# Performance work log

Measured on AMD Instinct MI355X. Metric: run time of the kernel, lower is better.

The kernel has to match this reference:

```python
import jax, jax.numpy as jnp
import numpy as np

B, N, EMBED, CHEB_K, INP, HID = 32, 8192, 16, 2, 2, 64


def setup_inputs() -> dict:
    key = jax.random.key(0)
    k1, k2, k3, k4 = jax.random.split(key, 4)
    return {
        "x": jax.random.normal(k1, (B, N, INP), dtype=jnp.float32),
        "adj": jax.random.normal(k2, (N, EMBED), dtype=jnp.float32),
        "weights_pool": jax.random.normal(k3, (EMBED, CHEB_K, INP, HID), dtype=jnp.float32) * 0.1,
        "bias_pool": jax.random.normal(k4, (EMBED, HID), dtype=jnp.float32) * 0.1,
    }


def reference(x, adj, weights_pool, bias_pool):
    n = adj.shape[0]
    cheb_k = weights_pool.shape[1]
    # adaptive adjacency: row-softmax of relu(E E^T)
    ADJ = jax.nn.softmax(jax.nn.relu(adj @ adj.T), axis=1)  # [n, n]
    support_set = [jnp.eye(n, dtype=x.dtype), ADJ]
    for k in range(2, cheb_k):  # Chebyshev recursion (fixed small k)
        support_set.append(2.0 * ADJ @ support_set[-1] - support_set[-2])
    supports = jnp.stack(support_set, axis=0)  # [k, n, n]
    # node-adaptive weights / bias
    weights = jnp.einsum("nd,dkio->nkio", adj, weights_pool)  # [n,k,inp,hid]
    bias = adj @ bias_pool  # [n, hid]
    # graph propagation, directly in bnkc layout (fuses the permute)
    x_g = jnp.einsum("knm,bmc->bnkc", supports, x)  # [b,n,k,inp]
    out = jnp.einsum("bnki,nkio->bno", x_g, weights) + bias  # [b,n,hid]
    return out
```

## Files before the change

kernel.cpp:

```cpp
#include <hip/hip_runtime.h>

#define NN 8192
#define BB 32
#define EMB 16
#define HID 64

typedef __attribute__((ext_vector_type(8))) short bf16x8;
typedef __attribute__((ext_vector_type(4))) float f32x4;

static __device__ inline unsigned short f2b(float f) {
    union { float f; unsigned u; } v; v.f = f;
    return (unsigned short)((v.u + 0x7fffu + ((v.u >> 16) & 1u)) >> 16);
}

static __device__ inline unsigned packbf(unsigned e_even, unsigned e_odd) {
#if __has_builtin(__builtin_amdgcn_perm)
    return __builtin_amdgcn_perm(e_odd, e_even, 0x07060302u);
#else
    return (e_odd & 0xFFFF0000u) | (e_even >> 16);
#endif
}

__global__ void k_build(const float* __restrict__ x, const float* __restrict__ adj,
                        const float* __restrict__ wp, const float* __restrict__ bp,
                        short* __restrict__ VTf, short* __restrict__ Afrag,
                        short* __restrict__ adjS, unsigned short* __restrict__ WbufB) {
    const int t = threadIdx.x;
    const int bx = blockIdx.x;
    if (bx < 256) {
        const int c = bx;
        const int u = t >> 6, lane = t & 63, l = lane & 15, q = lane >> 4;
        const int j = 16 * u + l, b = j >> 1, ch = j & 1;
        const int m0 = 32 * c + 8 * q;
        const float* xp = x + (size_t)b * (NN * 2) + m0 * 2;
        uint4 d;
        unsigned dd[4];
#pragma unroll
        for (int i = 0; i < 4; ++i) {
            float4 xx = *(const float4*)(xp + 4 * i);
            float v0 = ch ? xx.y : xx.x;
            float v1 = ch ? xx.w : xx.z;
            dd[i] = (unsigned)f2b(v0) | ((unsigned)f2b(v1) << 16);
        }
        d.x = dd[0]; d.y = dd[1]; d.z = dd[2]; d.w = dd[3];
        *(uint4*)(VTf + ((size_t)(c * 4 + u) * 64 + lane) * 8) = d;
    } else if (bx < 384) {
        const int cc = t >> 7, tt = t & 127;
        const int c = (bx - 256) * 2 + cc;
        const int h = tt >> 6, lane = tt & 63, l = lane & 15, q = lane >> 4;
        const int row = 32 * c + 8 * (l >> 2) + (l & 3) + 4 * h;
        const float* ap = adj + (size_t)row * EMB + (q & 1) * 8;
        float4 a0 = *(const float4*)(ap);
        float4 a1 = *(const float4*)(ap + 4);
        uint4 d;
        d.x = (unsigned)f2b(a0.x) | ((unsigned)f2b(a0.y) << 16);
        d.y = (unsigned)f2b(a0.z) | ((unsigned)f2b(a0.w) << 16);
        d.z = (unsigned)f2b(a1.x) | ((unsigned)f2b(a1.y) << 16);
        d.w = (unsigned)f2b(a1.z) | ((unsigned)f2b(a1.w) << 16);
        *(uint4*)(Afrag + ((size_t)(c * 2 + h) * 64 + lane) * 8) = d;
    } else if (bx < 512) {
        const float L2E = 1.4426950408889634f;
        int idx = (bx - 384) * 256 + t;
        float4 aa = *(const float4*)(adj + (size_t)idx * 4);
        uint2 us;
        us.x = (unsigned)f2b(aa.x * L2E) | ((unsigned)f2b(aa.y * L2E) << 16);
        us.y = (unsigned)f2b(aa.z * L2E) | ((unsigned)f2b(aa.w * L2E) << 16);
        *(uint2*)(adjS + (size_t)idx * 4) = us;
    } else {
        const int nl = t >> 4, og = t & 15;
        const int n = (bx - 512) * 16 + nl;
        const float4* wp4 = (const float4*)wp;
        const float4* bp4 = (const float4*)bp;
        float an[EMB];
#pragma unroll
        for (int d = 0; d < EMB; ++d) an[d] = adj[n * EMB + d];
        float4 w[5];
#pragma unroll
        for (int c = 0; c < 5; ++c) { w[c].x = w[c].y = w[c].z = w[c].w = 0.f; }
#pragma unroll
        for (int d = 0; d < EMB; ++d) {
            float a = an[d];
#pragma unroll
            for (int c = 0; c < 4; ++c) {
                float4 p = wp4[(d * 4 + c) * 16 + og];
                w[c].x += a * p.x; w[c].y += a * p.y; w[c].z += a * p.z; w[c].w += a * p.w;
            }
            float4 pb = bp4[d * 16 + og];
            w[4].x += a * pb.x; w[4].y += a * pb.y; w[4].z += a * pb.z; w[4].w += a * pb.w;
        }
#pragma unroll
        for (int c = 0; c < 5; ++c) {
            ushort4 pk;
            pk.x = f2b(w[c].x); pk.y = f2b(w[c].y); pk.z = f2b(w[c].z); pk.w = f2b(w[c].w);
            *(ushort4*)(WbufB + (size_t)n * 320 + c * 64 + og * 4) = pk;
        }
    }
}

__launch_bounds__(512, 1)
__global__ void k_fused(const short* __restrict__ Afrag, const short* __restrict__ adjS,
                        const short* __restrict__ VTf,
                        const unsigned short* __restrict__ WbufB, const float* __restrict__ x,
                        float* __restrict__ out) {
    const int t = threadIdx.x;
    const int wv = t >> 6;
    const int lane = t & 63;
    const int l = lane & 15;
    const int q = lane >> 4;
    const int n0 = blockIdx.x * 32;
    const int cbeg = wv * 32;
    const int cend = cbeg + 32;

    __shared__ __align__(16) unsigned short ysl[8][32][68];
    __shared__ float dsl[8][32];
    __shared__ float xl[32][68];
    __shared__ float ylf[32][68];

    bf16x8 Bn[2];
    bf16x8 zv = {0, 0, 0, 0, 0, 0, 0, 0};
#pragma unroll
    for (int s = 0; s < 2; ++s) {
        const short* src = adjS + (size_t)(n0 + 16 * s + l) * EMB + (q & 1) * 8;
        bf16x8 v = *(const bf16x8*)src;
        Bn[s] = (q < 2) ? v : zv;
    }
    const short one = (short)0x3F80;
    bf16x8 ones = {one, one, one, one, one, one, one, one};

    f32x4 acc[4][2];
    f32x4 dacc[2];
#pragma unroll
    for (int u = 0; u < 4; ++u)
#pragma unroll
        for (int s = 0; s < 2; ++s) { acc[u][s][0] = acc[u][s][1] = acc[u][s][2] = acc[u][s][3] = 0.f; }
#pragma unroll
    for (int s = 0; s < 2; ++s) { dacc[s][0] = dacc[s][1] = dacc[s][2] = dacc[s][3] = 0.f; }

    const short* Ap = Afrag + (size_t)lane * 8;
    const short* Vp = VTf + (size_t)lane * 8;

    bf16x8 aCur0 = *(const bf16x8*)(Ap + (size_t)cbeg * 1024);
    bf16x8 aCur1 = *(const bf16x8*)(Ap + (size_t)cbeg * 1024 + 512);

    for (int cg = cbeg; cg < cend; ++cg) {
        bf16x8 v0 = *(const bf16x8*)(Vp + (size_t)cg * 2048);
        bf16x8 v1 = *(const bf16x8*)(Vp + (size_t)cg * 2048 + 512);
        bf16x8 v2 = *(const bf16x8*)(Vp + (size_t)cg * 2048 + 1024);
        bf16x8 v3 = *(const bf16x8*)(Vp + (size_t)cg * 2048 + 1536);
        const int cgn = (cg + 1 < cend) ? cg + 1 : cbeg;
        bf16x8 aN0 = *(const bf16x8*)(Ap + (size_t)cgn * 1024);
        bf16x8 aN1 = *(const bf16x8*)(Ap + (size_t)cgn * 1024 + 512);

        f32x4 z = {0.f, 0.f, 0.f, 0.f};
        f32x4 S0[2], S1[2];
#pragma unroll
        for (int s = 0; s < 2; ++s) {
            S0[s] = __builtin_amdgcn_mfma_f32_16x16x32_bf16(aCur0, Bn[s], z, 0, 0, 0);
            S1[s] = __builtin_amdgcn_mfma_f32_16x16x32_bf16(aCur1, Bn[s], z, 0, 0, 0);
        }
#pragma unroll
        for (int s = 0; s < 2; ++s) {
            unsigned w0[4], w1[4];
#pragma unroll
            for (int r = 0; r < 4; ++r) {
                union { float f; unsigned u; } p0, p1;
                p0.f = __builtin_amdgcn_exp2f(fmaxf(S0[s][r], 0.f));
                p1.f = __builtin_amdgcn_exp2f(fmaxf(S1[s][r], 0.f));
                w0[r] = p0.u;
                w1[r] = p1.u;
            }
            union { bf16x8 v; unsigned d[4]; } pf;
            pf.d[0] = packbf(w0[0], w0[1]);
            pf.d[1] = packbf(w0[2], w0[3]);
            pf.d[2] = packbf(w1[0], w1[1]);
            pf.d[3] = packbf(w1[2], w1[3]);
            acc[0][s] = __builtin_amdgcn_mfma_f32_16x16x32_bf16(v0, pf.v, acc[0][s], 0, 0, 0);
            acc[1][s] = __builtin_amdgcn_mfma_f32_16x16x32_bf16(v1, pf.v, acc[1][s], 0, 0, 0);
            acc[2][s] = __builtin_amdgcn_mfma_f32_16x16x32_bf16(v2, pf.v, acc[2][s], 0, 0, 0);
            acc[3][s] = __builtin_amdgcn_mfma_f32_16x16x32_bf16(v3, pf.v, acc[3][s], 0, 0, 0);
            dacc[s] = __builtin_amdgcn_mfma_f32_16x16x32_bf16(ones, pf.v, dacc[s], 0, 0, 0);
        }
        aCur0 = aN0;
        aCur1 = aN1;
    }

#pragma unroll
    for (int s = 0; s < 2; ++s) {
        const int nl_w = 16 * s + l;
#pragma unroll
        for (int u = 0; u < 4; ++u) {
            union { float f; unsigned u; } a0, a1, a2, a3;
            a0.f = acc[u][s][0]; a1.f = acc[u][s][1]; a2.f = acc[u][s][2]; a3.f = acc[u][s][3];
            uint2 pk;
            pk.x = packbf(a0.u, a1.u);
            pk.y = packbf(a2.u, a3.u);
            *(uint2*)&ysl[wv][nl_w][16 * u + 4 * q] = pk;
        }
        if (q == 0) dsl[wv][nl_w] = dacc[s][0];
    }
    __syncthreads();

    const int nl = t >> 4, og = t & 15;
    const int n = n0 + nl;

    float4 W[5];
#pragma unroll
    for (int c = 0; c < 5; ++c) {
        ushort4 pw = *(const ushort4*)(WbufB + (size_t)n * 320 + c * 64 + og * 4);
        union { unsigned u; float f; } c0, c1, c2, c3;
        c0.u = (unsigned)pw.x << 16; c1.u = (unsigned)pw.y << 16;
        c2.u = (unsigned)pw.z << 16; c3.u = (unsigned)pw.w << 16;
        W[c].x = c0.f; W[c].y = c1.f; W[c].z = c2.f; W[c].w = c3.f;
    }

    float4 ysum; ysum.x = ysum.y = ysum.z = ysum.w = 0.f;
    float dsum = 0.f;
#pragma unroll
    for (int s = 0; s < 8; ++s) {
        ushort4 p = *(const ushort4*)&ysl[s][nl][og * 4];
        union { unsigned u; float f; } c0, c1, c2, c3;
        c0.u = (unsigned)p.x << 16; c1.u = (unsigned)p.y << 16;
        c2.u = (unsigned)p.z << 16; c3.u = (unsigned)p.w << 16;
        ysum.x += c0.f; ysum.y += c1.f; ysum.z += c2.f; ysum.w += c3.f;
        dsum += dsl[s][nl];
    }
    float rden = 1.f / dsum;
    *(float4*)&ylf[nl][og * 4] = make_float4(ysum.x * rden, ysum.y * rden, ysum.z * rden, ysum.w * rden);

    float2 x0 = *(const float2*)(x + ((size_t)(og * 2) * NN + n) * 2);
    float2 x1 = *(const float2*)(x + ((size_t)(og * 2 + 1) * NN + n) * 2);
    xl[nl][og * 4 + 0] = x0.x; xl[nl][og * 4 + 1] = x0.y;
    xl[nl][og * 4 + 2] = x1.x; xl[nl][og * 4 + 3] = x1.y;
    __syncthreads();

#pragma unroll 4
    for (int b = 0; b < BB; ++b) {
        float xb0 = xl[nl][2 * b], xb1 = xl[nl][2 * b + 1];
        float yb0 = ylf[nl][2 * b], yb1 = ylf[nl][2 * b + 1];
        f32x4 o4;
        o4[0] = xb0 * W[0].x + xb1 * W[1].x + yb0 * W[2].x + yb1 * W[3].x + W[4].x;
        o4[1] = xb0 * W[0].y + xb1 * W[1].y + yb0 * W[2].y + yb1 * W[3].y + W[4].y;
        o4[2] = xb0 * W[0].z + xb1 * W[1].z + yb0 * W[2].z + yb1 * W[3].z + W[4].z;
        o4[3] = xb0 * W[0].w + xb1 * W[1].w + yb0 * W[2].w + yb1 * W[3].w + W[4].w;
        __builtin_nontemporal_store(o4, (f32x4*)(out + ((size_t)b * NN + n) * HID + og * 4));
    }
}

extern "C" void kernel_launch(void* const* d_in, const int* in_sizes, int n_in,
                              void* d_out, int out_size, void* d_ws, size_t ws_size,
                              hipStream_t stream) {
    const float* x   = (const float*)d_in[0];
    const float* adj = (const float*)d_in[1];
    const float* wp  = (const float*)d_in[2];
    const float* bp  = (const float*)d_in[3];
    float* out = (float*)d_out;

    char* w = (char*)d_ws;
    short* VTf   = (short*)w;
    short* Afrag = VTf + (size_t)256 * 4 * 64 * 8;
    short* adjS  = Afrag + (size_t)256 * 2 * 64 * 8;
    unsigned short* WbufB = (unsigned short*)(adjS + (size_t)NN * EMB);

    k_build<<<1024, 256, 0, stream>>>(x, adj, wp, bp, VTf, Afrag, adjS, WbufB);
    k_fused<<<NN / 32, 512, 0, stream>>>(Afrag, adjS, VTf, WbufB, x, out);
}
```

Before: 116.5 us.

## Split attention over key halves with 64-node tiles and separate epilogue kernel

```diff
diff --git a/kernel.cpp b/kernel.cpp
--- a/kernel.cpp
+++ b/kernel.cpp
@@ -22,9 +22,8 @@
 }
 
 __global__ void k_build(const float* __restrict__ x, const float* __restrict__ adj,
-                        const float* __restrict__ wp, const float* __restrict__ bp,
                         short* __restrict__ VTf, short* __restrict__ Afrag,
-                        short* __restrict__ adjS, unsigned short* __restrict__ WbufB) {
+                        short* __restrict__ adjS) {
     const int t = threadIdx.x;
     const int bx = blockIdx.x;
     if (bx < 256) {
@@ -58,7 +57,7 @@
         d.z = (unsigned)f2b(a1.x) | ((unsigned)f2b(a1.y) << 16);
         d.w = (unsigned)f2b(a1.z) | ((unsigned)f2b(a1.w) << 16);
         *(uint4*)(Afrag + ((size_t)(c * 2 + h) * 64 + lane) * 8) = d;
-    } else if (bx < 512) {
+    } else {
         const float L2E = 1.4426950408889634f;
         int idx = (bx - 384) * 256 + t;
         float4 aa = *(const float4*)(adj + (size_t)idx * 4);
@@ -66,60 +65,31 @@
         us.x = (unsigned)f2b(aa.x * L2E) | ((unsigned)f2b(aa.y * L2E) << 16);
         us.y = (unsigned)f2b(aa.z * L2E) | ((unsigned)f2b(aa.w * L2E) << 16);
         *(uint2*)(adjS + (size_t)idx * 4) = us;
-    } else {
-        const int nl = t >> 4, og = t & 15;
-        const int n = (bx - 512) * 16 + nl;
-        const float4* wp4 = (const float4*)wp;
-        const float4* bp4 = (const float4*)bp;
-        float an[EMB];
-#pragma unroll
-        for (int d = 0; d < EMB; ++d) an[d] = adj[n * EMB + d];
-        float4 w[5];
-#pragma unroll
-        for (int c = 0; c < 5; ++c) { w[c].x = w[c].y = w[c].z = w[c].w = 0.f; }
-#pragma unroll
-        for (int d = 0; d < EMB; ++d) {
-            float a = an[d];
-#pragma unroll
-            for (int c = 0; c < 4; ++c) {
-                float4 p = wp4[(d * 4 + c) * 16 + og];
-                w[c].x += a * p.x; w[c].y += a * p.y; w[c].z += a * p.z; w[c].w += a * p.w;
-            }
-            float4 pb = bp4[d * 16 + og];
-            w[4].x += a * pb.x; w[4].y += a * pb.y; w[4].z += a * pb.z; w[4].w += a * pb.w;
-        }
-#pragma unroll
-        for (int c = 0; c < 5; ++c) {
-            ushort4 pk;
-            pk.x = f2b(w[c].x); pk.y = f2b(w[c].y); pk.z = f2b(w[c].z); pk.w = f2b(w[c].w);
-            *(ushort4*)(WbufB + (size_t)n * 320 + c * 64 + og * 4) = pk;
-        }
     }
 }
 
 __launch_bounds__(512, 1)
-__global__ void k_fused(const short* __restrict__ Afrag, const short* __restrict__ adjS,
-                        const short* __restrict__ VTf,
-                        const unsigned short* __restrict__ WbufB, const float* __restrict__ x,
-                        float* __restrict__ out) {
+__global__ void k_main(const short* __restrict__ Afrag, const short* __restrict__ adjS,
+                       const short* __restrict__ VTf,
+                       float* __restrict__ gnum, float* __restrict__ gden) {
     const int t = threadIdx.x;
     const int wv = t >> 6;
     const int lane = t & 63;
     const int l = lane & 15;
     const int q = lane >> 4;
-    const int n0 = blockIdx.x * 32;
-    const int cbeg = wv * 32;
-    const int cend = cbeg + 32;
-
-    __shared__ __align__(16) unsigned short ysl[8][32][68];
-    __shared__ float dsl[8][32];
-    __shared__ float xl[32][68];
-    __shared__ float ylf[32][68];
-
-    bf16x8 Bn[2];
+    const int tile = blockIdx.x & 127;
+    const int mh = blockIdx.x >> 7;
+    const int n0 = tile * 64;
+    const int cbeg = mh * 128 + wv * 16;
+    const int cend = cbeg + 16;
+
+    __shared__ __align__(16) unsigned short ysl[8][64][68];
+    __shared__ float dsl[8][64];
+
+    bf16x8 Bn[4];
     bf16x8 zv = {0, 0, 0, 0, 0, 0, 0, 0};
 #pragma unroll
-    for (int s = 0; s < 2; ++s) {
+    for (int s = 0; s < 4; ++s) {
         const short* src = adjS + (size_t)(n0 + 16 * s + l) * EMB + (q & 1) * 8;
         bf16x8 v = *(const bf16x8*)src;
         Bn[s] = (q < 2) ? v : zv;
@@ -127,14 +97,14 @@
     const short one = (short)0x3F80;
     bf16x8 ones = {one, one, one, one, one, one, one, one};
 
-    f32x4 acc[4][2];
-    f32x4 dacc[2];
+    f32x4 acc[4][4];
+    f32x4 dacc[4];
 #pragma unroll
     for (int u = 0; u < 4; ++u)
 #pragma unroll
-        for (int s = 0; s < 2; ++s) { acc[u][s][0] = acc[u][s][1] = acc[u][s][2] = acc[u][s][3] = 0.f; }
-#pragma unroll
-    for (int s = 0; s < 2; ++s) { dacc[s][0] = dacc[s][1] = dacc[s][2] = dacc[s][3] = 0.f; }
+        for (int s = 0; s < 4; ++s) { acc[u][s][0] = acc[u][s][1] = acc[u][s][2] = acc[u][s][3] = 0.f; }
+#pragma unroll
+    for (int s = 0; s < 4; ++s) { dacc[s][0] = dacc[s][1] = dacc[s][2] = dacc[s][3] = 0.f; }
 
     const short* Ap = Afrag + (size_t)lane * 8;
     const short* Vp = VTf + (size_t)lane * 8;
@@ -152,14 +122,14 @@
         bf16x8 aN1 = *(const bf16x8*)(Ap + (size_t)cgn * 1024 + 512);
 
         f32x4 z = {0.f, 0.f, 0.f, 0.f};
-        f32x4 S0[2], S1[2];
-#pragma unroll
-        for (int s = 0; s < 2; ++s) {
+        f32x4 S0[4], S1[4];
+#pragma unroll
+        for (int s = 0; s < 4; ++s) {
             S0[s] = __builtin_amdgcn_mfma_f32_16x16x32_bf16(aCur0, Bn[s], z, 0, 0, 0);
             S1[s] = __builtin_amdgcn_mfma_f32_16x16x32_bf16(aCur1, Bn[s], z, 0, 0, 0);
         }
 #pragma unroll
-        for (int s = 0; s < 2; ++s) {
+        for (int s = 0; s < 4; ++s) {
             unsigned w0[4], w1[4];
 #pragma unroll
             for (int r = 0; r < 4; ++r) {
@@ -185,7 +155,7 @@
     }
 
 #pragma unroll
-    for (int s = 0; s < 2; ++s) {
+    for (int s = 0; s < 4; ++s) {
         const int nl_w = 16 * s + l;
 #pragma unroll
         for (int u = 0; u < 4; ++u) {
@@ -200,38 +170,80 @@
     }
     __syncthreads();
 
+    float* gn = gnum + (size_t)(mh * 128 + tile) * 64 * 64;
+    float* gd = gden + (size_t)(mh * 128 + tile) * 64;
     const int nl = t >> 4, og = t & 15;
+#pragma unroll
+    for (int h = 0; h < 2; ++h) {
+        const int nr = nl + 32 * h;
+        f32x4 ysum = {0.f, 0.f, 0.f, 0.f};
+        float dsum = 0.f;
+#pragma unroll
+        for (int s = 0; s < 8; ++s) {
+            ushort4 p = *(const ushort4*)&ysl[s][nr][og * 4];
+            union { unsigned u; float f; } c0, c1, c2, c3;
+            c0.u = (unsigned)p.x << 16; c1.u = (unsigned)p.y << 16;
+            c2.u = (unsigned)p.z << 16; c3.u = (unsigned)p.w << 16;
+            ysum[0] += c0.f; ysum[1] += c1.f; ysum[2] += c2.f; ysum[3] += c3.f;
+            dsum += dsl[s][nr];
+        }
+        *(f32x4*)(gn + (size_t)nr * 64 + og * 4) = ysum;
+        if (og == 0) gd[nr] = dsum;
+    }
+}
+
+__global__ void k_epi2(const float* __restrict__ adj, const float* __restrict__ wp,
+                       const float* __restrict__ bp, const float* __restrict__ x,
+                       const float* __restrict__ gnum, const float* __restrict__ gden,
+                       float* __restrict__ out) {
+    const int t = threadIdx.x;
+    const int nl = t >> 4, og = t & 15;
+    const int tile = blockIdx.x >> 1;
+    const int half = blockIdx.x & 1;
+    const int n0 = blockIdx.x * 32;
+    const int nloc = half * 32 + nl;
     const int n = n0 + nl;
 
+    __shared__ float wpl[EMB][5][64];
+    __shared__ float adjl[32][EMB];
+    __shared__ float xl[32][68];
+    __shared__ float ylf[32][68];
+
+    for (int i = t; i < EMB * 5 * 64; i += 512) {
+        const int d = i / 320, r = i % 320, c = r >> 6, j = r & 63;
+        wpl[d][c][j] = (c < 4) ? wp[(size_t)(d * 4 + c) * 64 + j] : bp[(size_t)d * 64 + j];
+    }
+    adjl[nl][og] = adj[(size_t)(n0 + nl) * EMB + og];
+
+    const float* gn0 = gnum + (size_t)tile * 64 * 64;
+    const float* gn1 = gnum + (size_t)(128 + tile) * 64 * 64;
+    f32x4 y0 = *(const f32x4*)(gn0 + (size_t)nloc * 64 + og * 4);
+    f32x4 y1 = *(const f32x4*)(gn1 + (size_t)nloc * 64 + og * 4);
+    float dsum = gden[(size_t)tile * 64 + nloc] + gden[(size_t)(128 + tile) * 64 + nloc];
+    float rden = 1.f / dsum;
+    ylf[nl][og * 4 + 0] = (y0[0] + y1[0]) * rden;
+    ylf[nl][og * 4 + 1] = (y0[1] + y1[1]) * rden;
+    ylf[nl][og * 4 + 2] = (y0[2] + y1[2]) * rden;
+    ylf[nl][og * 4 + 3] = (y0[3] + y1[3]) * rden;
+
+    float2 x0 = *(const float2*)(x + ((size_t)(og * 2) * NN + n) * 2);
+    float2 x1v = *(const float2*)(x + ((size_t)(og * 2 + 1) * NN + n) * 2);
+    xl[nl][og * 4 + 0] = x0.x; xl[nl][og * 4 + 1] = x0.y;
+    xl[nl][og * 4 + 2] = x1v.x; xl[nl][og * 4 + 3] = x1v.y;
+    __syncthreads();
+
     float4 W[5];
 #pragma unroll
-    for (int c = 0; c < 5; ++c) {
-        ushort4 pw = *(const ushort4*)(WbufB + (size_t)n * 320 + c * 64 + og * 4);
-        union { unsigned u; float f; } c0, c1, c2, c3;
-        c0.u = (unsigned)pw.x << 16; c1.u = (unsigned)pw.y << 16;
-        c2.u = (unsigned)pw.z << 16; c3.u = (unsigned)pw.w << 16;
-        W[c].x = c0.f; W[c].y = c1.f; W[c].z = c2.f; W[c].w = c3.f;
-    }
-
-    float4 ysum; ysum.x = ysum.y = ysum.z = ysum.w = 0.f;
-    float dsum = 0.f;
-#pragma unroll
-    for (int s = 0; s < 8; ++s) {
-        ushort4 p = *(const ushort4*)&ysl[s][nl][og * 4];
-        union { unsigned u; float f; } c0, c1, c2, c3;
-        c0.u = (unsigned)p.x << 16; c1.u = (unsigned)p.y << 16;
-        c2.u = (unsigned)p.z << 16; c3.u = (unsigned)p.w << 16;
-        ysum.x += c0.f; ysum.y += c1.f; ysum.z += c2.f; ysum.w += c3.f;
-        dsum += dsl[s][nl];
-    }
-    float rden = 1.f / dsum;
-    *(float4*)&ylf[nl][og * 4] = make_float4(ysum.x * rden, ysum.y * rden, ysum.z * rden, ysum.w * rden);
-
-    float2 x0 = *(const float2*)(x + ((size_t)(og * 2) * NN + n) * 2);
-    float2 x1 = *(const float2*)(x + ((size_t)(og * 2 + 1) * NN + n) * 2);
-    xl[nl][og * 4 + 0] = x0.x; xl[nl][og * 4 + 1] = x0.y;
-    xl[nl][og * 4 + 2] = x1.x; xl[nl][og * 4 + 3] = x1.y;
-    __syncthreads();
+    for (int c = 0; c < 5; ++c) { W[c].x = W[c].y = W[c].z = W[c].w = 0.f; }
+#pragma unroll
+    for (int d = 0; d < EMB; ++d) {
+        const float a = adjl[nl][d];
+#pragma unroll
+        for (int c = 0; c < 5; ++c) {
+            const float4 p = *(const float4*)&wpl[d][c][og * 4];
+            W[c].x += a * p.x; W[c].y += a * p.y; W[c].z += a * p.z; W[c].w += a * p.w;
+        }
+    }
 
 #pragma unroll 4
     for (int b = 0; b < BB; ++b) {
@@ -259,8 +271,10 @@
     short* VTf   = (short*)w;
     short* Afrag = VTf + (size_t)256 * 4 * 64 * 8;
     short* adjS  = Afrag + (size_t)256 * 2 * 64 * 8;
-    unsigned short* WbufB = (unsigned short*)(adjS + (size_t)NN * EMB);
-
-    k_build<<<1024, 256, 0, stream>>>(x, adj, wp, bp, VTf, Afrag, adjS, WbufB);
-    k_fused<<<NN / 32, 512, 0, stream>>>(Afrag, adjS, VTf, WbufB, x, out);
-}
+    float* gnum  = (float*)(adjS + (size_t)NN * EMB);
+    float* gden  = gnum + (size_t)256 * 64 * 64;
+
+    k_build<<<512, 256, 0, stream>>>(x, adj, VTf, Afrag, adjS);
+    k_main<<<256, 512, 0, stream>>>(Afrag, adjS, VTf, gnum, gden);
+    k_epi2<<<256, 512, 0, stream>>>(adj, wp, bp, x, gnum, gden, out);
+}
```

New measurement: 111.4 us. 4.3% less time.
